# Performance work log

Measured on AMD Instinct MI355X. Metric: run time of the kernel, lower is better.

## Reference

```python
import jax, jax.numpy as jnp
import numpy as np

N, E, B, D, H, L = 50000, 800000, 16, 64, 128, 2


def _lin(h, w, b):
    return h @ w + b


def _scatter_mean(v, idx, n):
    s = jax.ops.segment_sum(v, idx, num_segments=n)
    c = jax.ops.segment_sum(jnp.ones((v.shape[0],), v.dtype), idx, num_segments=n)
    return s / jnp.maximum(c, 1.0)[:, None]


def setup_inputs() -> dict:
    key = jax.random.key(0)
    ks = iter(jax.random.split(key, 40))

    def p(*shape):
        return jax.random.normal(next(ks), shape, dtype=jnp.float32) * 0.05

    inp = {
        "x": jax.random.normal(next(ks), (N, D), dtype=jnp.float32),
        "edge_attr": jax.random.normal(next(ks), (E, D), dtype=jnp.float32),
        "u": jax.random.normal(next(ks), (B, D), dtype=jnp.float32),
        "e_w1": p(L, 4 * D, H), "e_b1": p(L, H),
        "e_w2": p(L, H, H), "e_b2": p(L, H),
        "e_w3": p(L, H, D), "e_b3": p(L, D),
        "n1_w1": p(L, 2 * D, H), "n1_b1": p(L, H),
        "n1_w2": p(L, H, H), "n1_b2": p(L, H),
        "n2_w1": p(L, D + H + D, H), "n2_b1": p(L, H),
        "n2_w2": p(L, H, D), "n2_b2": p(L, D),
        "g_w1": p(L, 3 * D, H), "g_b1": p(L, H),
        "g_w2": p(L, H, D), "g_b2": p(L, D),
        "edge_index": jax.random.randint(next(ks), (2, E), 0, N, dtype=jnp.int32),
        "batch": jnp.sort(jax.random.randint(next(ks), (N,), 0, B, dtype=jnp.int32)),
    }
    return inp


def _forward(x, edge_attr, u, params, edge_index, batch):
    row, col = edge_index[0], edge_index[1]
    eb = batch[row]  # [E] graph id per edge
    x0, e0, u0 = x, edge_attr, u
    for l in range(L):
        (e_w1, e_b1, e_w2, e_b2, e_w3, e_b3,
         n1_w1, n1_b1, n1_w2, n1_b2,
         n2_w1, n2_b1, n2_w2, n2_b2,
         g_w1, g_b1, g_w2, g_b2) = [pm[l] for pm in params]
        # Edge model: [E, e+2n+u] -> MLP -> [E, D]
        h = jnp.concatenate([x[row], x[col], edge_attr, u[eb]], axis=1)
        h = jax.nn.relu(_lin(h, e_w1, e_b1))
        h = jax.nn.relu(_lin(h, e_w2, e_b2))
        edge_attr = _lin(h, e_w3, e_b3)
        # Node model: gather src node + edge, MLP1, scatter_mean onto dest, MLP2
        se = jnp.concatenate([x[row], edge_attr], axis=1)  # [E, 2D]
        se = _lin(jax.nn.relu(_lin(se, n1_w1, n1_b1)), n1_w2, n1_b2)
        agg = _scatter_mean(se, col, N)  # [N, H]
        xh = jnp.concatenate([x, agg, u[batch]], axis=1)
        x = _lin(jax.nn.relu(_lin(xh, n2_w1, n2_b1)), n2_w2, n2_b2)
        # Global model: per-graph means of updated nodes/edges
        e_agg = _scatter_mean(edge_attr, eb, B)
        n_agg = _scatter_mean(x, batch, B)
        uh = jnp.concatenate([u, n_agg, e_agg], axis=1)
        u = _lin(jax.nn.relu(_lin(uh, g_w1, g_b1)), g_w2, g_b2)
    return x + x0, edge_attr + e0, u + u0


def reference(x, edge_attr, u, e_w1, e_b1, e_w2, e_b2, e_w3, e_b3, n1_w1, n1_b1, n1_w2, n1_b2, n2_w1, n2_b1, n2_w2, n2_b2, g_w1, g_b1, g_w2, g_b2, edge_index, batch):
    params = (e_w1, e_b1, e_w2, e_b2, e_w3, e_b3,
              n1_w1, n1_b1, n1_w2, n1_b2,
              n2_w1, n2_b1, n2_w2, n2_b2,
              g_w1, g_b1, g_w2, g_b2)
    return _forward(x, edge_attr, u, params, edge_index, batch)
```

## Files before the change

### kernel.cpp

```cpp
#include <hip/hip_runtime.h>

#define N_NODES 50000
#define E_EDGES 800000
#define NG 16
#define DD 64
#define HH 128
#define NB_SCAN 49

typedef __attribute__((ext_vector_type(8))) __bf16 bf16x8;
typedef __attribute__((ext_vector_type(4))) float f32x4;
typedef unsigned int uint;
typedef unsigned short ushort;
typedef __attribute__((ext_vector_type(4))) uint uint4v;

#define MFMA16(a,b,c) __builtin_amdgcn_mfma_f32_16x16x32_bf16((a),(b),(c),0,0,0)

__device__ __forceinline__ ushort f2bf(float f){
  uint u = __builtin_bit_cast(uint, f);
  u += 0x7fffu + ((u >> 16) & 1u);
  return (ushort)(u >> 16);
}
__device__ __forceinline__ uint pk2(float a, float b){
  return (uint)f2bf(a) | ((uint)f2bf(b) << 16);
}
__device__ __forceinline__ float bflo(uint u){ return __builtin_bit_cast(float, u << 16); }
__device__ __forceinline__ float bfhi(uint u){ return __builtin_bit_cast(float, u & 0xffff0000u); }

__device__ __forceinline__ bf16x8 ldfrag(const char* base, int row, int byteoff){
  uint4v v = *(const uint4v*)(base + row*256 + (byteoff ^ ((row & 7) << 4)));
  return __builtin_bit_cast(bf16x8, v);
}
__device__ __forceinline__ uint4v ld_chunk(const char* base, int row, int c16){
  return *(const uint4v*)(base + row*256 + ((c16*16) ^ ((row & 7) << 4)));
}
__device__ __forceinline__ void st_h(char* base, int row, int col, float v){
  *(ushort*)(base + row*256 + ((col*2) ^ ((row & 7) << 4))) = f2bf(v);
}
__device__ __forceinline__ void st_chunk(char* base, int row, int c16, uint4v v){
  *(uint4v*)(base + row*256 + ((c16*16) ^ ((row & 7) << 4))) = v;
}
__device__ __forceinline__ bf16x8 ldfrag128(const char* base, int row, int byteoff){
  uint4v v = *(const uint4v*)(base + row*128 + (byteoff ^ ((row & 7) << 4)));
  return __builtin_bit_cast(bf16x8, v);
}
__device__ __forceinline__ void st_chunk128(char* base, int row, int c16, uint4v v){
  *(uint4v*)(base + row*128 + ((c16*16) ^ ((row & 7) << 4))) = v;
}
__device__ __forceinline__ void pack16_128(char* dst, int r, int c16, const float* src){
  float4 lo = *(const float4*)src;
  float4 hi = *(const float4*)(src + 4);
  uint4v v; v.x = pk2(lo.x, lo.y); v.y = pk2(lo.z, lo.w);
  v.z = pk2(hi.x, hi.y); v.w = pk2(hi.z, hi.w);
  st_chunk128(dst, r, c16, v);
}

__device__ __forceinline__ void stage_b(char* sB, const ushort* wt,
                                        int Nout, int Ktot, int koff, int t, int stride){
  for (int task = t; task < Nout*16; task += stride){
    int n = task >> 4, c = task & 15;
    uint4v v = *(const uint4v*)(wt + (long)n*Ktot + koff + c*8);
    st_chunk(sB, n, c, v);
  }
}
__device__ __forceinline__ void pack16(char* dst, int r, int c16, const float* src){
  float4 lo = *(const float4*)src;
  float4 hi = *(const float4*)(src + 4);
  uint4v v; v.x = pk2(lo.x, lo.y); v.y = pk2(lo.z, lo.w);
  v.z = pk2(hi.x, hi.y); v.w = pk2(hi.z, hi.w);
  st_chunk(dst, r, c16, v);
}
template<int NT>
__device__ __forceinline__ void gemm_acc(const char* A, const char* B,
                                         int wv, int l15, int lhi, f32x4* acc){
  #pragma unroll
  for (int kt = 0; kt < 4; ++kt){
    bf16x8 a = ldfrag(A, wv*16 + l15, kt*64 + lhi*16);
    #pragma unroll
    for (int n = 0; n < NT; ++n){
      bf16x8 bb = ldfrag(B, n*16 + l15, kt*64 + lhi*16);
      acc[n] = MFMA16(a, bb, acc[n]);
    }
  }
}
template<int NT, bool RELU>
__device__ __forceinline__ void epi_lds(char* dst, const f32x4* acc, const float* bias,
                                        int wv, int l15, int lhi){
  #pragma unroll
  for (int n = 0; n < NT; ++n){
    float bv = bias[n*16 + l15];
    #pragma unroll
    for (int j = 0; j < 4; ++j){
      int r = wv*16 + lhi*4 + j;
      float v = acc[n][j] + bv;
      if (RELU) v = fmaxf(v, 0.f);
      st_h(dst, r, n*16 + l15, v);
    }
  }
}

__global__ void pack_weights(const float* __restrict__ e1, const float* __restrict__ e2,
                             const float* __restrict__ e3, const float* __restrict__ n12,
                             const float* __restrict__ n21, const float* __restrict__ n22,
                             ushort* __restrict__ out){
  int idx = blockIdx.x * 256 + threadIdx.x;
  int l = idx / 114688, r = idx % 114688;
  const float* src; int K, N, off;
  if      (r <  32768){ src = e1;  K = 256; N = 128; off = 0; }
  else if (r <  49152){ src = e2;  K = 128; N = 128; off = 32768; }
  else if (r <  57344){ src = e3;  K = 128; N = 64;  off = 49152; }
  else if (r <  73728){ src = n12; K = 128; N = 128; off = 57344; }
  else if (r < 106496){ src = n21; K = 256; N = 128; off = 73728; }
  else                { src = n22; K = 128; N = 64;  off = 106496; }
  int q = r - off; int k = q / N; int n = q % N;
  out[(long)l*139264 + off + n*K + k] = f2bf(src[(long)l*K*N + q]);
}

__global__ void make_wc(const float* __restrict__ n1w1, const float* __restrict__ ew3,
                        const float* __restrict__ n1b1, const float* __restrict__ eb3,
                        ushort* __restrict__ packed, float* __restrict__ biasc){
  int l = blockIdx.x, t = threadIdx.x;
  const float* W1 = n1w1 + (long)l*128*128;
  const float* W3 = ew3 + (long)l*128*64;
  ushort* wc = packed + (long)l*139264 + 114688;
  for (int i = t; i < 8192; i += 256){
    int k = i >> 7, n = i & 127;
    wc[n*192 + k] = f2bf(W1[k*128 + n]);
  }
  for (int i = t; i < 16384; i += 256){
    int k2 = i >> 7, n = i & 127;
    float s = 0.f;
    for (int m = 0; m < 64; ++m) s += W3[k2*64 + m] * W1[(64 + m)*128 + n];
    wc[n*192 + 64 + k2] = f2bf(s);
  }
  if (t < 128){
    float s = n1b1[l*128 + t];
    for (int m = 0; m < 64; ++m) s += eb3[l*64 + m] * W1[(64 + m)*128 + t];
    biasc[l*128 + t] = s;
  }
}

__global__ void hist_kernel(const int* __restrict__ edge_index, const int* __restrict__ batch,
                            int* __restrict__ deg, float* __restrict__ cnt_eb){
  __shared__ float h[NG];
  int t = threadIdx.x;
  if (t < NG) h[t] = 0.f;
  __syncthreads();
  int e = blockIdx.x * 256 + t;
  if (e < E_EDGES){
    atomicAdd(deg + edge_index[E_EDGES + e], 1);
    atomicAdd(&h[batch[edge_index[e]]], 1.f);
  }
  __syncthreads();
  if (t < NG) atomicAdd(cnt_eb + t, h[t]);
}
__global__ void count_nodes_kernel(const int* __restrict__ batch, float* __restrict__ cnt_b){
  __shared__ float h[NG];
  int t = threadIdx.x;
  if (t < NG) h[t] = 0.f;
  __syncthreads();
  int n = blockIdx.x * 256 + t;
  if (n < N_NODES) atomicAdd(&h[batch[n]], 1.f);
  __syncthreads();
  if (t < NG) atomicAdd(cnt_b + t, h[t]);
}
__global__ void scan_a(const int* __restrict__ deg, int* __restrict__ bsum){
  __shared__ int red[1024];
  int i = blockIdx.x*1024 + threadIdx.x;
  red[threadIdx.x] = (i < N_NODES) ? deg[i] : 0;
  __syncthreads();
  for (int s = 512; s > 0; s >>= 1){
    if ((int)threadIdx.x < s) red[threadIdx.x] += red[threadIdx.x + s];
    __syncthreads();
  }
  if (threadIdx.x == 0) bsum[blockIdx.x] = red[0];
}
__global__ void scan_b(const int* __restrict__ bsum, int* __restrict__ bbase){
  if (threadIdx.x == 0){
    int run = 0;
    for (int b = 0; b < NB_SCAN; ++b){ int v = bsum[b]; bbase[b] = run; run += v; }
  }
}
__global__ void scan_c(const int* __restrict__ deg, const int* __restrict__ bbase,
                       int* __restrict__ off, int* __restrict__ cursor){
  __shared__ int sc[1024];
  int i = blockIdx.x*1024 + threadIdx.x;
  int v = (i < N_NODES) ? deg[i] : 0;
  sc[threadIdx.x] = v;
  __syncthreads();
  for (int d = 1; d < 1024; d <<= 1){
    int add = ((int)threadIdx.x >= d) ? sc[threadIdx.x - d] : 0;
    __syncthreads();
    sc[threadIdx.x] += add;
    __syncthreads();
  }
  if (i < N_NODES){
    int ex = sc[threadIdx.x] - v + bbase[blockIdx.x];
    off[i] = ex; cursor[i] = ex;
  }
}
__global__ void fill_kernel(const int* __restrict__ edge_index, int* __restrict__ cursor,
                            int* __restrict__ pos){
  int e = blockIdx.x*256 + threadIdx.x;
  if (e < E_EDGES){
    int c = edge_index[E_EDGES + e];
    pos[e] = atomicAdd(&cursor[c], 1);
  }
}

__global__ __launch_bounds__(256, 3) void k123_kernel(
    const float* __restrict__ x_cur, const float* e_cur,
    const float* __restrict__ u_cur,
    const int* __restrict__ ei, const int* __restrict__ batch,
    const ushort* __restrict__ w1t, const ushort* __restrict__ w2t,
    const float* __restrict__ be1, const float* __restrict__ be2,
    ushort* h2g)
{
  __shared__ __align__(16) char lds[49152];
  __shared__ int sRow[128], sCol[128], sEb[128];
  char* A  = lds;
  char* B  = lds + 16384;
  char* OV = lds + 16384;
  const int t = threadIdx.x;
  const int wv = t >> 6, l15 = t & 15, lhi = (t >> 4) & 3;
  const int ebase = blockIdx.x * 128;

  if (t < 128){
    int r = ei[ebase + t];
    sRow[t] = r; sCol[t] = ei[E_EDGES + ebase + t]; sEb[t] = batch[r];
  }
  __syncthreads();

  f32x4 acc[2][8];
  #pragma unroll
  for (int m = 0; m < 2; ++m)
    #pragma unroll
    for (int n = 0; n < 8; ++n) acc[m][n] = f32x4{0,0,0,0};

  for (int c = 0; c < 4; ++c){
    #pragma unroll
    for (int it = 0; it < 4; ++it){
      int task = t + it*256, r = task >> 3, c16 = task & 7;
      const float* s;
      if      (c == 0) s = x_cur + (long)sRow[r]*DD + c16*8;
      else if (c == 1) s = x_cur + (long)sCol[r]*DD + c16*8;
      else if (c == 2) s = e_cur + (long)(ebase + r)*DD + c16*8;
      else             s = u_cur + (long)sEb[r]*DD + c16*8;
      pack16_128(A, r, c16, s);
    }
    #pragma unroll
    for (int it = 0; it < 4; ++it){
      int task = t + it*256, n = task >> 3, c16 = task & 7;
      st_chunk128(B, n, c16, *(const uint4v*)(w1t + (long)n*256 + c*64 + c16*8));
    }
    __syncthreads();
    #pragma unroll
    for (int kt = 0; kt < 2; ++kt){
      bf16x8 a0 = ldfrag128(A, wv*32 + l15,      kt*64 + lhi*16);
      bf16x8 a1 = ldfrag128(A, wv*32 + 16 + l15, kt*64 + lhi*16);
      #pragma unroll
      for (int n = 0; n < 8; ++n){
        bf16x8 bb = ldfrag128(B, n*16 + l15, kt*64 + lhi*16);
        acc[0][n] = MFMA16(a0, bb, acc[0][n]);
        acc[1][n] = MFMA16(a1, bb, acc[1][n]);
      }
    }
    __syncthreads();
  }
  #pragma unroll
  for (int m = 0; m < 2; ++m)
    #pragma unroll
    for (int n = 0; n < 8; ++n){
      int col = n*16 + l15;
      float bv = be1[col];
      #pragma unroll
      for (int j = 0; j < 4; ++j)
        st_h(OV, wv*32 + m*16 + lhi*4 + j, col, fmaxf(acc[m][n][j] + bv, 0.f));
    }
  __syncthreads();

  #pragma unroll
  for (int m = 0; m < 2; ++m)
    #pragma unroll
    for (int n = 0; n < 8; ++n) acc[m][n] = f32x4{0,0,0,0};
  for (int kc = 0; kc < 2; ++kc){
    #pragma unroll
    for (int it = 0; it < 4; ++it){
      int task = t + it*256, n = task >> 3, c16 = task & 7;
      st_chunk128(A, n, c16, *(const uint4v*)(w2t + (long)n*128 + kc*64 + c16*8));
    }
    __syncthreads();
    #pragma unroll
    for (int kt = 0; kt < 2; ++kt){
      bf16x8 a0 = ldfrag(OV, wv*32 + l15,      kc*128 + kt*64 + lhi*16);
      bf16x8 a1 = ldfrag(OV, wv*32 + 16 + l15, kc*128 + kt*64 + lhi*16);
      #pragma unroll
      for (int n = 0; n < 8; ++n){
        bf16x8 bb = ldfrag128(A, n*16 + l15, kt*64 + lhi*16);
        acc[0][n] = MFMA16(a0, bb, acc[0][n]);
        acc[1][n] = MFMA16(a1, bb, acc[1][n]);
      }
    }
    __syncthreads();
  }
  #pragma unroll
  for (int m = 0; m < 2; ++m)
    #pragma unroll
    for (int n = 0; n < 8; ++n){
      int col = n*16 + l15;
      float bv = be2[col];
      #pragma unroll
      for (int j = 0; j < 4; ++j)
        st_h(OV, wv*32 + m*16 + lhi*4 + j, col, fmaxf(acc[m][n][j] + bv, 0.f));
    }
  __syncthreads();
  #pragma unroll
  for (int it = 0; it < 8; ++it){
    int task = t + it*256, r = task >> 4, c16 = task & 15;
    *(uint4v*)(h2g + (long)(ebase + r)*HH + c16*8) = ld_chunk(OV, r, c16);
  }
}

template<bool CSR>
__global__ __launch_bounds__(256, 3) void k45_kernel(
    const float* __restrict__ x_cur, const ushort* h2g,
    const int* __restrict__ ei, const int* __restrict__ batch,
    const int* __restrict__ pos_arr,
    const ushort* __restrict__ w3t, const ushort* __restrict__ wct,
    const ushort* __restrict__ w5t,
    const float* __restrict__ be3, const float* __restrict__ biasc,
    const float* __restrict__ bn12,
    float* e_outf, const float* __restrict__ e_resid,
    ushort* __restrict__ se_buf, float* __restrict__ agg_sum,
    float* __restrict__ e_agg, int has_resid)
{
  __shared__ __align__(16) char lds[49152];
  __shared__ float sEagg[NG*DD];
  __shared__ int sIdx[128];
  char* A  = lds;
  char* B  = lds + 16384;
  char* B2 = lds + 32768;
  char* OV = lds + 16384;
  const int t = threadIdx.x;
  const int wv = t >> 6, l15 = t & 15, lhi = (t >> 4) & 3;
  const int ebase = blockIdx.x * 128;

  if (t < 128) sIdx[t] = ei[ebase + t];
  for (int i = t; i < NG*DD; i += 256) sEagg[i] = 0.f;
  __syncthreads();

  f32x4 acc4[2][8], acc3[2][4];
  #pragma unroll
  for (int m = 0; m < 2; ++m){
    #pragma unroll
    for (int n = 0; n < 8; ++n) acc4[m][n] = f32x4{0,0,0,0};
    #pragma unroll
    for (int n = 0; n < 4; ++n) acc3[m][n] = f32x4{0,0,0,0};
  }

  for (int c = 0; c < 3; ++c){
    if (c == 0){
      #pragma unroll
      for (int it = 0; it < 4; ++it){
        int task = t + it*256, r = task >> 3, c16 = task & 7;
        pack16_128(A, r, c16, x_cur + (long)sIdx[r]*DD + c16*8);
      }
      #pragma unroll
      for (int it = 0; it < 4; ++it){
        int task = t + it*256, n = task >> 4, c16 = task & 15;
        st_chunk(B2, n, c16, *(const uint4v*)(w3t + (long)n*128 + c16*8));
      }
    } else {
      #pragma unroll
      for (int it = 0; it < 4; ++it){
        int task = t + it*256, r = task >> 3, c16 = task & 7;
        st_chunk128(A, r, c16,
            *(const uint4v*)(h2g + (long)(ebase + r)*HH + (c-1)*64 + c16*8));
      }
    }
    #pragma unroll
    for (int it = 0; it < 4; ++it){
      int task = t + it*256, n = task >> 3, c16 = task & 7;
      st_chunk128(B, n, c16, *(const uint4v*)(wct + (long)n*192 + c*64 + c16*8));
    }
    __syncthreads();
    #pragma unroll
    for (int kt = 0; kt < 2; ++kt){
      bf16x8 a0 = ldfrag128(A, wv*32 + l15,      kt*64 + lhi*16);
      bf16x8 a1 = ldfrag128(A, wv*32 + 16 + l15, kt*64 + lhi*16);
      #pragma unroll
      for (int n = 0; n < 8; ++n){
        bf16x8 bb = ldfrag128(B, n*16 + l15, kt*64 + lhi*16);
        acc4[0][n] = MFMA16(a0, bb, acc4[0][n]);
        acc4[1][n] = MFMA16(a1, bb, acc4[1][n]);
      }
      if (c >= 1){
        #pragma unroll
        for (int n = 0; n < 4; ++n){
          bf16x8 b2 = ldfrag(B2, n*16 + l15, (c-1)*128 + kt*64 + lhi*16);
          acc3[0][n] = MFMA16(a0, b2, acc3[0][n]);
          acc3[1][n] = MFMA16(a1, b2, acc3[1][n]);
        }
      }
    }
    __syncthreads();
  }

  #pragma unroll
  for (int m = 0; m < 2; ++m)
    #pragma unroll
    for (int n = 0; n < 4; ++n){
      int col = n*16 + l15;
      float bv = be3[col];
      #pragma unroll
      for (int j = 0; j < 4; ++j){
        int row = wv*32 + m*16 + lhi*4 + j;
        float v = acc3[m][n][j] + bv;
        long eg = (long)(ebase + row)*DD + col;
        e_outf[eg] = has_resid ? (v + e_resid[eg]) : v;
        int eb = batch[ei[ebase + row]];
        atomicAdd(&sEagg[eb*DD + col], v);
      }
    }
  #pragma unroll
  for (int m = 0; m < 2; ++m)
    #pragma unroll
    for (int n = 0; n < 8; ++n){
      int col = n*16 + l15;
      float bv = biasc[col];
      #pragma unroll
      for (int j = 0; j < 4; ++j)
        st_h(OV, wv*32 + m*16 + lhi*4 + j, col, fmaxf(acc4[m][n][j] + bv, 0.f));
    }
  #pragma unroll
  for (int it = 0; it < 4; ++it){
    int task = t + it*256, n = task >> 3, c16 = task & 7;
    st_chunk128(A, n, c16, *(const uint4v*)(w5t + (long)n*128 + c16*8));
  }
  if (t < 128) sIdx[t] = CSR ? pos_arr[ebase + t] : ei[E_EDGES + ebase + t];
  __syncthreads();

  f32x4 acc5[2][8];
  #pragma unroll
  for (int m = 0; m < 2; ++m)
    #pragma unroll
    for (int n = 0; n < 8; ++n) acc5[m][n] = f32x4{0,0,0,0};
  #pragma unroll
  for (int kt = 0; kt < 2; ++kt){
    bf16x8 a0 = ldfrag(OV, wv*32 + l15,      kt*64 + lhi*16);
    bf16x8 a1 = ldfrag(OV, wv*32 + 16 + l15, kt*64 + lhi*16);
    #pragma unroll
    for (int n = 0; n < 8; ++n){
      bf16x8 bb = ldfrag128(A, n*16 + l15, kt*64 + lhi*16);
      acc5[0][n] = MFMA16(a0, bb, acc5[0][n]);
      acc5[1][n] = MFMA16(a1, bb, acc5[1][n]);
    }
  }
  __syncthreads();
  #pragma unroll
  for (int it = 0; it < 4; ++it){
    int task = t + it*256, n = task >> 3, c16 = task & 7;
    st_chunk128(A, n, c16, *(const uint4v*)(w5t + (long)n*128 + 64 + c16*8));
  }
  __syncthreads();
  #pragma unroll
  for (int kt = 0; kt < 2; ++kt){
    bf16x8 a0 = ldfrag(OV, wv*32 + l15,      128 + kt*64 + lhi*16);
    bf16x8 a1 = ldfrag(OV, wv*32 + 16 + l15, 128 + kt*64 + lhi*16);
    #pragma unroll
    for (int n = 0; n < 8; ++n){
      bf16x8 bb = ldfrag128(A, n*16 + l15, kt*64 + lhi*16);
      acc5[0][n] = MFMA16(a0, bb, acc5[0][n]);
      acc5[1][n] = MFMA16(a1, bb, acc5[1][n]);
    }
  }
  __syncthreads();

  if (CSR){
    #pragma unroll
    for (int m = 0; m < 2; ++m)
      #pragma unroll
      for (int n = 0; n < 8; ++n){
        int col = n*16 + l15;
        float bv = bn12[col];
        #pragma unroll
        for (int j = 0; j < 4; ++j)
          st_h(OV, wv*32 + m*16 + lhi*4 + j, col, acc5[m][n][j] + bv);
      }
    __syncthreads();
    #pragma unroll
    for (int it = 0; it < 8; ++it){
      int task = t + it*256, r = task >> 4, c16 = task & 15;
      *(uint4v*)(se_buf + (long)sIdx[r]*HH + c16*8) = ld_chunk(OV, r, c16);
    }
  } else {
    #pragma unroll
    for (int m = 0; m < 2; ++m)
      #pragma unroll
      for (int n = 0; n < 8; ++n){
        int col = n*16 + l15;
        float bv = bn12[col];
        #pragma unroll
        for (int j = 0; j < 4; ++j){
          int row = wv*32 + m*16 + lhi*4 + j;
          atomicAdd(agg_sum + (long)sIdx[row]*HH + col, acc5[m][n][j] + bv);
        }
      }
    __syncthreads();
  }
  for (int i = t; i < NG*DD; i += 256) atomicAdd(e_agg + i, sEagg[i]);
}

template<bool CSR>
__global__ __launch_bounds__(256, 2) void node_kernel(
    const float* __restrict__ x_cur, const float* __restrict__ u_cur,
    const float* __restrict__ x_resid, const int* __restrict__ batch,
    const ushort* __restrict__ se_buf, const int* __restrict__ deg,
    const int* __restrict__ off, const float* __restrict__ agg_sum,
    const ushort* __restrict__ w_n21, const ushort* __restrict__ w_n22,
    const float* __restrict__ b_n21, const float* __restrict__ b_n22,
    float* __restrict__ x_out, float* __restrict__ n_agg, int has_resid)
{
  __shared__ __align__(16) char sA[16384];
  __shared__ __align__(16) char sB[32768];
  __shared__ __align__(16) char sH[16384];
  __shared__ int sBat[64], sDeg[64], sOff[64];
  __shared__ float sRinv[64];
  __shared__ float sNagg[NG*DD];

  const int t = threadIdx.x;
  const int wv = t >> 6, ln = t & 63, l15 = ln & 15, lhi = ln >> 4;
  const int n0 = blockIdx.x * 64;

  if (t < 64){
    int nd = n0 + t;
    int ok = nd < N_NODES;
    sBat[t] = ok ? batch[nd] : 0;
    int d = ok ? deg[nd] : 0;
    sDeg[t] = d;
    sOff[t] = ok ? off[nd] : 0;
    sRinv[t] = 1.f / fmaxf((float)d, 1.f);
  }
  for (int i = t; i < NG*DD; i += 256) sNagg[i] = 0.f;
  __syncthreads();

  float s[32];
  const int r4 = t >> 2, q = t & 3;
  if (CSR){
    #pragma unroll
    for (int k = 0; k < 32; ++k) s[k] = 0.f;
    int d = sDeg[r4], o = sOff[r4];
    for (int i = 0; i < d; ++i){
      const ushort* src = se_buf + (long)(o + i)*HH + q*32;
      #pragma unroll
      for (int c = 0; c < 4; ++c){
        uint4v v = *(const uint4v*)(src + c*8);
        #pragma unroll
        for (int jj = 0; jj < 4; ++jj){
          s[c*8 + jj*2]     += bflo(v[jj]);
          s[c*8 + jj*2 + 1] += bfhi(v[jj]);
        }
      }
    }
    float riv = sRinv[r4];
    #pragma unroll
    for (int k = 0; k < 32; ++k) s[k] *= riv;
  }

  f32x4 acc[8];
  #pragma unroll
  for (int n = 0; n < 8; ++n) acc[n] = f32x4{0.f,0.f,0.f,0.f};

  for (int half = 0; half < 2; ++half){
    if (CSR){
      for (int task = t; task < 512; task += 256){
        int r = task >> 3, c = task & 7;
        int nd = n0 + r;
        bool ok = nd < N_NODES;
        float4 lo = {0,0,0,0}, hi = {0,0,0,0};
        if (ok){
          const float* src = (half == 0) ? (x_cur + (long)nd*DD + c*8)
                                         : (u_cur + (long)sBat[r]*DD + c*8);
          lo = *(const float4*)src; hi = *(const float4*)(src + 4);
        }
        uint4v v; v.x = pk2(lo.x, lo.y); v.y = pk2(lo.z, lo.w);
        v.z = pk2(hi.x, hi.y); v.w = pk2(hi.z, hi.w);
        st_chunk(sA, r, (half == 0) ? c : (8 + c), v);
      }
      if ((half == 0 && q < 2) || (half == 1 && q >= 2)){
        int cbase = (half == 0) ? (8 + q*4) : ((q - 2)*4);
        #pragma unroll
        for (int cc = 0; cc < 4; ++cc){
          uint4v v;
          v.x = pk2(s[cc*8+0], s[cc*8+1]); v.y = pk2(s[cc*8+2], s[cc*8+3]);
          v.z = pk2(s[cc*8+4], s[cc*8+5]); v.w = pk2(s[cc*8+6], s[cc*8+7]);
          st_chunk(sA, r4, cbase + cc, v);
        }
      }
    } else {
      for (int task = t; task < 1024; task += 256){
        int r = task >> 4, c = task & 15;
        int nd = n0 + r;
        bool ok = nd < N_NODES;
        float scale = 1.f;
        const float* src;
        if (half == 0){
          if (c < 8) src = x_cur + (long)nd*DD + c*8;
          else { src = agg_sum + (long)nd*HH + (c-8)*8; scale = sRinv[r]; }
        } else {
          if (c < 8){ src = agg_sum + (long)nd*HH + 64 + c*8; scale = sRinv[r]; }
          else src = u_cur + (long)sBat[r]*DD + (c-8)*8;
        }
        float4 lo = {0,0,0,0}, hi = {0,0,0,0};
        if (ok){ lo = *(const float4*)src; hi = *(const float4*)(src + 4); }
        uint4v v; v.x = pk2(lo.x*scale, lo.y*scale); v.y = pk2(lo.z*scale, lo.w*scale);
        v.z = pk2(hi.x*scale, hi.y*scale); v.w = pk2(hi.z*scale, hi.w*scale);
        st_chunk(sA, r, c, v);
      }
    }
    stage_b(sB, w_n21, 128, 256, half*128, t, 256);
    __syncthreads();
    gemm_acc<8>(sA, sB, wv, l15, lhi, acc);
    __syncthreads();
  }
  epi_lds<8, true>(sH, acc, b_n21, wv, l15, lhi);
  stage_b(sB, w_n22, 64, 128, 0, t, 256);
  __syncthreads();

  f32x4 acc2[4];
  #pragma unroll
  for (int n = 0; n < 4; ++n) acc2[n] = f32x4{0.f,0.f,0.f,0.f};
  gemm_acc<4>(sH, sB, wv, l15, lhi, acc2);

  #pragma unroll
  for (int n = 0; n < 4; ++n){
    float bv = b_n22[n*16 + l15];
    #pragma unroll
    for (int j = 0; j < 4; ++j){
      int r = wv*16 + lhi*4 + j;
      int nd = n0 + r;
      if (nd < N_NODES){
        int col = n*16 + l15;
        float v = acc2[n][j] + bv;
        long xg = (long)nd*DD + col;
        x_out[xg] = has_resid ? (v + x_resid[xg]) : v;
        atomicAdd(&sNagg[sBat[r]*DD + col], v);
      }
    }
  }
  __syncthreads();
  for (int i = t; i < NG*DD; i += 256) atomicAdd(n_agg + i, sNagg[i]);
}

__global__ void global_kernel(const float* __restrict__ u_cur, const float* __restrict__ n_agg,
                              const float* __restrict__ e_agg, const float* __restrict__ cnt_b,
                              const float* __restrict__ cnt_e,
                              const float* __restrict__ g_w1, const float* __restrict__ g_b1,
                              const float* __restrict__ g_w2, const float* __restrict__ g_b2,
                              const float* __restrict__ u_resid, float* __restrict__ u_out,
                              int has_resid)
{
// ... 127 lines not shown
```

Before: 1.910 ms.

## Prefetch next K-chunk into registers and use lgkm-only barriers in edge kernels

The two edge-path kernels now load the next gathered activation chunk and weight chunk from global memory into registers while the current chunk's MFMA work runs. They also replace __syncthreads with a barrier that waits only on LDS counters, so outstanding global loads can stay in flight across the barrier. The k45 kernel precomputes the edge's graph id and destination index into shared memory once, instead of re-reading batch[ei[...]] per element in the epilogue, and drops some redundant barriers. The trade-off is higher register pressure from the prefetch buffers, which may reduce occupancy under the launch bounds. The weaker barrier is also a correctness risk if any global-to-LDS dependency relied on the full sync; packing row | batch<<16 assumes node ids fit in 16 bits, and N=50000 does.

```diff
diff --git a/kernel.cpp b/kernel.cpp
--- a/kernel.cpp
+++ b/kernel.cpp
@@ -26,6 +26,11 @@
 __device__ __forceinline__ float bflo(uint u){ return __builtin_bit_cast(float, u << 16); }
 __device__ __forceinline__ float bfhi(uint u){ return __builtin_bit_cast(float, u & 0xffff0000u); }
 
+__device__ __forceinline__ void lds_barrier(){
+  asm volatile("s_waitcnt lgkmcnt(0)" ::: "memory");
+  __builtin_amdgcn_s_barrier();
+}
+
 __device__ __forceinline__ bf16x8 ldfrag(const char* base, int row, int byteoff){
   uint4v v = *(const uint4v*)(base + row*256 + (byteoff ^ ((row & 7) << 4)));
   return __builtin_bit_cast(bf16x8, v);
@@ -45,13 +50,6 @@
 }
 __device__ __forceinline__ void st_chunk128(char* base, int row, int c16, uint4v v){
   *(uint4v*)(base + row*128 + ((c16*16) ^ ((row & 7) << 4))) = v;
-}
-__device__ __forceinline__ void pack16_128(char* dst, int r, int c16, const float* src){
-  float4 lo = *(const float4*)src;
-  float4 hi = *(const float4*)(src + 4);
-  uint4v v; v.x = pk2(lo.x, lo.y); v.y = pk2(lo.z, lo.w);
-  v.z = pk2(hi.x, hi.y); v.w = pk2(hi.z, hi.w);
-  st_chunk128(dst, r, c16, v);
 }
 
 __device__ __forceinline__ void stage_b(char* sB, const ushort* wt,
@@ -61,13 +59,6 @@
     uint4v v = *(const uint4v*)(wt + (long)n*Ktot + koff + c*8);
     st_chunk(sB, n, c, v);
   }
-}
-__device__ __forceinline__ void pack16(char* dst, int r, int c16, const float* src){
-  float4 lo = *(const float4*)src;
-  float4 hi = *(const float4*)(src + 4);
-  uint4v v; v.x = pk2(lo.x, lo.y); v.y = pk2(lo.z, lo.w);
-  v.z = pk2(hi.x, hi.y); v.w = pk2(hi.z, hi.w);
-  st_chunk(dst, r, c16, v);
 }
 template<int NT>
 __device__ __forceinline__ void gemm_acc(const char* A, const char* B,
@@ -230,13 +221,9 @@
   }
   __syncthreads();
 
-  f32x4 acc[2][8];
-  #pragma unroll
-  for (int m = 0; m < 2; ++m)
-    #pragma unroll
-    for (int n = 0; n < 8; ++n) acc[m][n] = f32x4{0,0,0,0};
-
-  for (int c = 0; c < 4; ++c){
+  float4 gr[8];
+  uint4v wr[4];
+  auto GLOAD = [&](int c){
     #pragma unroll
     for (int it = 0; it < 4; ++it){
       int task = t + it*256, r = task >> 3, c16 = task & 7;
@@ -245,14 +232,55 @@
       else if (c == 1) s = x_cur + (long)sCol[r]*DD + c16*8;
       else if (c == 2) s = e_cur + (long)(ebase + r)*DD + c16*8;
       else             s = u_cur + (long)sEb[r]*DD + c16*8;
-      pack16_128(A, r, c16, s);
-    }
+      gr[2*it] = *(const float4*)s; gr[2*it+1] = *(const float4*)(s + 4);
+    }
+  };
+  auto ASTORE = [&](){
+    #pragma unroll
+    for (int it = 0; it < 4; ++it){
+      int task = t + it*256, r = task >> 3, c16 = task & 7;
+      uint4v v;
+      v.x = pk2(gr[2*it].x, gr[2*it].y);     v.y = pk2(gr[2*it].z, gr[2*it].w);
+      v.z = pk2(gr[2*it+1].x, gr[2*it+1].y); v.w = pk2(gr[2*it+1].z, gr[2*it+1].w);
+      st_chunk128(A, r, c16, v);
+    }
+  };
+  auto W1LOAD = [&](int c){
     #pragma unroll
     for (int it = 0; it < 4; ++it){
       int task = t + it*256, n = task >> 3, c16 = task & 7;
-      st_chunk128(B, n, c16, *(const uint4v*)(w1t + (long)n*256 + c*64 + c16*8));
-    }
-    __syncthreads();
+      wr[it] = *(const uint4v*)(w1t + (long)n*256 + c*64 + c16*8);
+    }
+  };
+  auto W2LOAD = [&](int kc){
+    #pragma unroll
+    for (int it = 0; it < 4; ++it){
+      int task = t + it*256, n = task >> 3, c16 = task & 7;
+      wr[it] = *(const uint4v*)(w2t + (long)n*128 + kc*64 + c16*8);
+    }
+  };
+  auto BSTORE = [&](char* dst){
+    #pragma unroll
+    for (int it = 0; it < 4; ++it){
+      int task = t + it*256, n = task >> 3, c16 = task & 7;
+      st_chunk128(dst, n, c16, wr[it]);
+    }
+  };
+
+  f32x4 acc[2][8];
+  #pragma unroll
+  for (int m = 0; m < 2; ++m)
+    #pragma unroll
+    for (int n = 0; n < 8; ++n) acc[m][n] = f32x4{0,0,0,0};
+
+  GLOAD(0); W1LOAD(0);
+
+  #pragma unroll
+  for (int c = 0; c < 4; ++c){
+    ASTORE(); BSTORE(B);
+    if (c < 3){ GLOAD(c + 1); W1LOAD(c + 1); }
+    else      { W2LOAD(0); }
+    lds_barrier();
     #pragma unroll
     for (int kt = 0; kt < 2; ++kt){
       bf16x8 a0 = ldfrag128(A, wv*32 + l15,      kt*64 + lhi*16);
@@ -264,7 +292,7 @@
         acc[1][n] = MFMA16(a1, bb, acc[1][n]);
       }
     }
-    __syncthreads();
+    lds_barrier();
   }
   #pragma unroll
   for (int m = 0; m < 2; ++m)
@@ -276,19 +304,16 @@
       for (int j = 0; j < 4; ++j)
         st_h(OV, wv*32 + m*16 + lhi*4 + j, col, fmaxf(acc[m][n][j] + bv, 0.f));
     }
-  __syncthreads();
 
   #pragma unroll
   for (int m = 0; m < 2; ++m)
     #pragma unroll
     for (int n = 0; n < 8; ++n) acc[m][n] = f32x4{0,0,0,0};
+  #pragma unroll
   for (int kc = 0; kc < 2; ++kc){
-    #pragma unroll
-    for (int it = 0; it < 4; ++it){
-      int task = t + it*256, n = task >> 3, c16 = task & 7;
-      st_chunk128(A, n, c16, *(const uint4v*)(w2t + (long)n*128 + kc*64 + c16*8));
-    }
-    __syncthreads();
+    BSTORE(A);
+    if (kc == 0) W2LOAD(1);
+    lds_barrier();
     #pragma unroll
     for (int kt = 0; kt < 2; ++kt){
       bf16x8 a0 = ldfrag(OV, wv*32 + l15,      kc*128 + kt*64 + lhi*16);
@@ -300,7 +325,7 @@
         acc[1][n] = MFMA16(a1, bb, acc[1][n]);
       }
     }
-    __syncthreads();
+    lds_barrier();
   }
   #pragma unroll
   for (int m = 0; m < 2; ++m)
@@ -312,7 +337,7 @@
       for (int j = 0; j < 4; ++j)
         st_h(OV, wv*32 + m*16 + lhi*4 + j, col, fmaxf(acc[m][n][j] + bv, 0.f));
     }
-  __syncthreads();
+  lds_barrier();
   #pragma unroll
   for (int it = 0; it < 8; ++it){
     int task = t + it*256, r = task >> 4, c16 = task & 15;
@@ -335,7 +360,8 @@
 {
   __shared__ __align__(16) char lds[49152];
   __shared__ float sEagg[NG*DD];
-  __shared__ int sIdx[128];
+  __shared__ int sRow[128];
+  __shared__ int sDst[128];
   char* A  = lds;
   char* B  = lds + 16384;
   char* B2 = lds + 32768;
@@ -344,10 +370,91 @@
   const int wv = t >> 6, l15 = t & 15, lhi = (t >> 4) & 3;
   const int ebase = blockIdx.x * 128;
 
-  if (t < 128) sIdx[t] = ei[ebase + t];
+  if (t < 128){
+    int r = ei[ebase + t];
+    sDst[t] = CSR ? pos_arr[ebase + t] : ei[E_EDGES + ebase + t];
+    sRow[t] = r | (batch[r] << 16);
+  }
   for (int i = t; i < NG*DD; i += 256) sEagg[i] = 0.f;
   __syncthreads();
 
+  float4 gr[8];
+  uint4v hr[4], wr[4], b2r[4];
+  auto GLOADX = [&](){
+    #pragma unroll
+    for (int it = 0; it < 4; ++it){
+      int task = t + it*256, r = task >> 3, c16 = task & 7;
+      const float* s = x_cur + (long)(sRow[r] & 0xffff)*DD + c16*8;
+      gr[2*it] = *(const float4*)s; gr[2*it+1] = *(const float4*)(s + 4);
+    }
+  };
+  auto ASTOREX = [&](){
+    #pragma unroll
+    for (int it = 0; it < 4; ++it){
+      int task = t + it*256, r = task >> 3, c16 = task & 7;
+      uint4v v;
+      v.x = pk2(gr[2*it].x, gr[2*it].y);     v.y = pk2(gr[2*it].z, gr[2*it].w);
+      v.z = pk2(gr[2*it+1].x, gr[2*it+1].y); v.w = pk2(gr[2*it+1].z, gr[2*it+1].w);
+      st_chunk128(A, r, c16, v);
+    }
+  };
+  auto HLOAD = [&](int half){
+    #pragma unroll
+    for (int it = 0; it < 4; ++it){
+      int task = t + it*256, r = task >> 3, c16 = task & 7;
+      hr[it] = *(const uint4v*)(h2g + (long)(ebase + r)*HH + half*64 + c16*8);
+    }
+  };
+  auto ASTOREH = [&](){
+    #pragma unroll
+    for (int it = 0; it < 4; ++it){
+      int task = t + it*256, r = task >> 3, c16 = task & 7;
+      st_chunk128(A, r, c16, hr[it]);
+    }
+  };
+  auto WCLOAD = [&](int c){
+    #pragma unroll
+    for (int it = 0; it < 4; ++it){
+      int task = t + it*256, n = task >> 3, c16 = task & 7;
+      wr[it] = *(const uint4v*)(wct + (long)n*192 + c*64 + c16*8);
+    }
+  };
+  auto W5LOAD = [&](int kc){
+    #pragma unroll
+    for (int it = 0; it < 4; ++it){
+      int task = t + it*256, n = task >> 3, c16 = task & 7;
+      wr[it] = *(const uint4v*)(w5t + (long)n*128 + kc*64 + c16*8);
+    }
+  };
+  auto WSTORE = [&](){
+    #pragma unroll
+    for (int it = 0; it < 4; ++it){
+      int task = t + it*256, n = task >> 3, c16 = task & 7;
+      st_chunk128(B, n, c16, wr[it]);
+    }
+  };
+  auto WSTORE_A = [&](){
+    #pragma unroll
+    for (int it = 0; it < 4; ++it){
+      int task = t + it*256, n = task >> 3, c16 = task & 7;
+      st_chunk128(A, n, c16, wr[it]);
+    }
+  };
+  auto B2LOAD = [&](){
+    #pragma unroll
+    for (int it = 0; it < 4; ++it){
+      int task = t + it*256, n = task >> 4, c16 = task & 15;
+      b2r[it] = *(const uint4v*)(w3t + (long)n*128 + c16*8);
+    }
+  };
+  auto B2STORE = [&](){
+    #pragma unroll
+    for (int it = 0; it < 4; ++it){
+      int task = t + it*256, n = task >> 4, c16 = task & 15;
+      st_chunk(B2, n, c16, b2r[it]);
+    }
+  };
+
   f32x4 acc4[2][8], acc3[2][4];
   #pragma unroll
   for (int m = 0; m < 2; ++m){
@@ -357,32 +464,17 @@
     for (int n = 0; n < 4; ++n) acc3[m][n] = f32x4{0,0,0,0};
   }
 
+  GLOADX(); WCLOAD(0); B2LOAD();
+
+  #pragma unroll
   for (int c = 0; c < 3; ++c){
-    if (c == 0){
-      #pragma unroll
-      for (int it = 0; it < 4; ++it){
-        int task = t + it*256, r = task >> 3, c16 = task & 7;
-        pack16_128(A, r, c16, x_cur + (long)sIdx[r]*DD + c16*8);
-      }
-      #pragma unroll
-      for (int it = 0; it < 4; ++it){
-        int task = t + it*256, n = task >> 4, c16 = task & 15;
-        st_chunk(B2, n, c16, *(const uint4v*)(w3t + (long)n*128 + c16*8));
-      }
-    } else {
-      #pragma unroll
-      for (int it = 0; it < 4; ++it){
-        int task = t + it*256, r = task >> 3, c16 = task & 7;
-        st_chunk128(A, r, c16,
-            *(const uint4v*)(h2g + (long)(ebase + r)*HH + (c-1)*64 + c16*8));
-      }
-    }
-    #pragma unroll
-    for (int it = 0; it < 4; ++it){
-      int task = t + it*256, n = task >> 3, c16 = task & 7;
-      st_chunk128(B, n, c16, *(const uint4v*)(wct + (long)n*192 + c*64 + c16*8));
-    }
-    __syncthreads();
+    if (c == 0){ ASTOREX(); B2STORE(); }
+    else       { ASTOREH(); }
+    WSTORE();
+    if (c == 0){ HLOAD(0); WCLOAD(1); }
+    else if (c == 1){ HLOAD(1); WCLOAD(2); }
+    else { W5LOAD(0); }
+    lds_barrier();
     #pragma unroll
     for (int kt = 0; kt < 2; ++kt){
       bf16x8 a0 = ldfrag128(A, wv*32 + l15,      kt*64 + lhi*16);
@@ -402,7 +494,7 @@
         }
       }
     }
-    __syncthreads();
+    lds_barrier();
   }
 
   #pragma unroll
@@ -417,8 +509,7 @@
         float v = acc3[m][n][j] + bv;
         long eg = (long)(ebase + row)*DD + col;
         e_outf[eg] = has_resid ? (v + e_resid[eg]) : v;
-        int eb = batch[ei[ebase + row]];
-        atomicAdd(&sEagg[eb*DD + col], v);
+        atomicAdd(&sEagg[(sRow[row] >> 16)*DD + col], v);
       }
     }
   #pragma unroll
@@ -431,13 +522,6 @@
       for (int j = 0; j < 4; ++j)
         st_h(OV, wv*32 + m*16 + lhi*4 + j, col, fmaxf(acc4[m][n][j] + bv, 0.f));
     }
-  #pragma unroll
-  for (int it = 0; it < 4; ++it){
-    int task = t + it*256, n = task >> 3, c16 = task & 7;
-    st_chunk128(A, n, c16, *(const uint4v*)(w5t + (long)n*128 + c16*8));
-  }
-  if (t < 128) sIdx[t] = CSR ? pos_arr[ebase + t] : ei[E_EDGES + ebase + t];
-  __syncthreads();
 
   f32x4 acc5[2][8];
   #pragma unroll
@@ -445,35 +529,23 @@
     #pragma unroll
     for (int n = 0; n < 8; ++n) acc5[m][n] = f32x4{0,0,0,0};
   #pragma unroll
-  for (int kt = 0; kt < 2; ++kt){
-    bf16x8 a0 = ldfrag(OV, wv*32 + l15,      kt*64 + lhi*16);
-    bf16x8 a1 = ldfrag(OV, wv*32 + 16 + l15, kt*64 + lhi*16);
-    #pragma unroll
-    for (int n = 0; n < 8; ++n){
-      bf16x8 bb = ldfrag128(A, n*16 + l15, kt*64 + lhi*16);
-      acc5[0][n] = MFMA16(a0, bb, acc5[0][n]);
-      acc5[1][n] = MFMA16(a1, bb, acc5[1][n]);
-    }
-  }
-  __syncthreads();
-  #pragma unroll
-  for (int it = 0; it < 4; ++it){
-    int task = t + it*256, n = task >> 3, c16 = task & 7;
-    st_chunk128(A, n, c16, *(const uint4v*)(w5t + (long)n*128 + 64 + c16*8));
-  }
-  __syncthreads();
-  #pragma unroll
-  for (int kt = 0; kt < 2; ++kt){
-    bf16x8 a0 = ldfrag(OV, wv*32 + l15,      128 + kt*64 + lhi*16);
-    bf16x8 a1 = ldfrag(OV, wv*32 + 16 + l15, 128 + kt*64 + lhi*16);
-    #pragma unroll
-    for (int n = 0; n < 8; ++n){
-      bf16x8 bb = ldfrag128(A, n*16 + l15, kt*64 + lhi*16);
-      acc5[0][n] = MFMA16(a0, bb, acc5[0][n]);
-      acc5[1][n] = MFMA16(a1, bb, acc5[1][n]);
-    }
-  }
-  __syncthreads();
+  for (int kc = 0; kc < 2; ++kc){
+    WSTORE_A();
+    if (kc == 0) W5LOAD(1);
+    lds_barrier();
+    #pragma unroll
+    for (int kt = 0; kt < 2; ++kt){
+      bf16x8 a0 = ldfrag(OV, wv*32 + l15,      kc*128 + kt*64 + lhi*16);
+      bf16x8 a1 = ldfrag(OV, wv*32 + 16 + l15, kc*128 + kt*64 + lhi*16);
+      #pragma unroll
+      for (int n = 0; n < 8; ++n){
+        bf16x8 bb = ldfrag128(A, n*16 + l15, kt*64 + lhi*16);
+        acc5[0][n] = MFMA16(a0, bb, acc5[0][n]);
+        acc5[1][n] = MFMA16(a1, bb, acc5[1][n]);
+      }
+    }
+    lds_barrier();
+  }
 
   if (CSR){
     #pragma unroll
@@ -486,11 +558,11 @@
         for (int j = 0; j < 4; ++j)
           st_h(OV, wv*32 + m*16 + lhi*4 + j, col, acc5[m][n][j] + bv);
       }
-    __syncthreads();
+    lds_barrier();
     #pragma unroll
     for (int it = 0; it < 8; ++it){
       int task = t + it*256, r = task >> 4, c16 = task & 15;
-      *(uint4v*)(se_buf + (long)sIdx[r]*HH + c16*8) = ld_chunk(OV, r, c16);
+      *(uint4v*)(se_buf + (long)sDst[r]*HH + c16*8) = ld_chunk(OV, r, c16);
     }
   } else {
     #pragma unroll
@@ -502,7 +574,7 @@
         #pragma unroll
         for (int j = 0; j < 4; ++j){
           int row = wv*32 + m*16 + lhi*4 + j;
-          atomicAdd(agg_sum + (long)sIdx[row]*HH + col, acc5[m][n][j] + bv);
+          atomicAdd(agg_sum + (long)sDst[row]*HH + col, acc5[m][n][j] + bv);
         }
       }
     __syncthreads();
```

New measurement: 2.001 ms. 4.7% more time.

## Pipeline k45 kernel loads via async global_load_lds with multi-slot LDS staging

Applied to the files above, without the earlier changes.

Restructures the fused edge/node-MLP kernel so weight and h2 tiles are loaded straight into LDS with asynchronous global_load_lds into four 16KB slots, overlapping the loads with the MFMA phases through explicit vmcnt waits and raw barriers. The e_w3 weights move into registers instead of LDS, and the source-node batch id is packed into the row index so the scatter no longer does a second indirect load. LDS grows to 64KB and occupancy drops from 3 to 2 blocks per CU, which may offset the latency hiding. The hand-placed waitcnt and barrier sequencing is fragile.

```diff
diff --git a/kernel.cpp b/kernel.cpp
--- a/kernel.cpp
+++ b/kernel.cpp
@@ -26,6 +26,18 @@
 __device__ __forceinline__ float bflo(uint u){ return __builtin_bit_cast(float, u << 16); }
 __device__ __forceinline__ float bfhi(uint u){ return __builtin_bit_cast(float, u & 0xffff0000u); }
 
+__device__ __forceinline__ void bar(){
+  asm volatile("s_waitcnt lgkmcnt(0)" ::: "memory");
+  __builtin_amdgcn_s_barrier();
+}
+#define VMWAIT(n) asm volatile("s_waitcnt vmcnt(" #n ")" ::: "memory")
+
+__device__ __forceinline__ void gload16(const void* g, void* l){
+  __builtin_amdgcn_global_load_lds(
+      (const __attribute__((address_space(1))) unsigned int*)g,
+      (__attribute__((address_space(3))) unsigned int*)l, 16, 0, 0);
+}
+
 __device__ __forceinline__ bf16x8 ldfrag(const char* base, int row, int byteoff){
   uint4v v = *(const uint4v*)(base + row*256 + (byteoff ^ ((row & 7) << 4)));
   return __builtin_bit_cast(bf16x8, v);
@@ -61,13 +73,6 @@
     uint4v v = *(const uint4v*)(wt + (long)n*Ktot + koff + c*8);
     st_chunk(sB, n, c, v);
   }
-}
-__device__ __forceinline__ void pack16(char* dst, int r, int c16, const float* src){
-  float4 lo = *(const float4*)src;
-  float4 hi = *(const float4*)(src + 4);
-  uint4v v; v.x = pk2(lo.x, lo.y); v.y = pk2(lo.z, lo.w);
-  v.z = pk2(hi.x, hi.y); v.w = pk2(hi.z, hi.w);
-  st_chunk(dst, r, c16, v);
 }
 template<int NT>
 __device__ __forceinline__ void gemm_acc(const char* A, const char* B,
@@ -321,7 +326,7 @@
 }
 
 template<bool CSR>
-__global__ __launch_bounds__(256, 3) void k45_kernel(
+__global__ __launch_bounds__(256, 2) void k45_kernel(
     const float* __restrict__ x_cur, const ushort* h2g,
     const int* __restrict__ ei, const int* __restrict__ batch,
     const int* __restrict__ pos_arr,
@@ -333,21 +338,54 @@
     ushort* __restrict__ se_buf, float* __restrict__ agg_sum,
     float* __restrict__ e_agg, int has_resid)
 {
-  __shared__ __align__(16) char lds[49152];
+  __shared__ __align__(16) char lds[65536];
   __shared__ float sEagg[NG*DD];
-  __shared__ int sIdx[128];
-  char* A  = lds;
-  char* B  = lds + 16384;
-  char* B2 = lds + 32768;
-  char* OV = lds + 16384;
+  __shared__ int sRow[128];
+  __shared__ int sDst[128];
+  char* S0 = lds;
+  char* S1 = lds + 16384;
+  char* S2 = lds + 32768;
+  char* S3 = lds + 49152;
+  char* OV = lds;
+  char* SE = lds + 32768;
   const int t = threadIdx.x;
-  const int wv = t >> 6, l15 = t & 15, lhi = (t >> 4) & 3;
+  const int wv = t >> 6, lane = t & 63, l15 = t & 15, lhi = (t >> 4) & 3;
   const int ebase = blockIdx.x * 128;
 
-  if (t < 128) sIdx[t] = ei[ebase + t];
+  auto GL = [&](const ushort* base, long stride, int koff, char* slot){
+    #pragma unroll
+    for (int it = 0; it < 4; ++it){
+      int q = (wv*4 + it)*64 + lane;
+      int r = q >> 3, cp = q & 7;
+      gload16(base + (long)r*stride + koff + ((cp ^ (r & 7))*8),
+              slot + (wv*4 + it)*1024);
+    }
+  };
+
+  if (t < 128){
+    int r = ei[ebase + t];
+    sDst[t] = CSR ? pos_arr[ebase + t] : ei[E_EDGES + ebase + t];
+    sRow[t] = r | (batch[r] << 16);
+  }
+  GL(wct, 192, 0, S1);
+  GL(h2g + (long)ebase*HH, HH, 0, S2);
+  GL(wct, 192, 64, S3);
+  bf16x8 b3[4][4];
+  #pragma unroll
+  for (int n = 0; n < 4; ++n)
+    #pragma unroll
+    for (int kk = 0; kk < 4; ++kk)
+      b3[n][kk] = *(const bf16x8*)(w3t + (long)(n*16 + l15)*128 + kk*32 + lhi*8);
   for (int i = t; i < NG*DD; i += 256) sEagg[i] = 0.f;
   __syncthreads();
 
+  #pragma unroll
+  for (int it = 0; it < 4; ++it){
+    int task = t + it*256, r = task >> 3, c16 = task & 7;
+    pack16_128(S0, r, c16, x_cur + (long)(sRow[r] & 0xffff)*DD + c16*8);
+  }
+  __syncthreads();
+
   f32x4 acc4[2][8], acc3[2][4];
   #pragma unroll
   for (int m = 0; m < 2; ++m){
@@ -357,32 +395,7 @@
     for (int n = 0; n < 4; ++n) acc3[m][n] = f32x4{0,0,0,0};
   }
 
-  for (int c = 0; c < 3; ++c){
-    if (c == 0){
-      #pragma unroll
-      for (int it = 0; it < 4; ++it){
-        int task = t + it*256, r = task >> 3, c16 = task & 7;
-        pack16_128(A, r, c16, x_cur + (long)sIdx[r]*DD + c16*8);
-      }
-      #pragma unroll
-      for (int it = 0; it < 4; ++it){
-        int task = t + it*256, n = task >> 4, c16 = task & 15;
-        st_chunk(B2, n, c16, *(const uint4v*)(w3t + (long)n*128 + c16*8));
-      }
-    } else {
-      #pragma unroll
-      for (int it = 0; it < 4; ++it){
-        int task = t + it*256, r = task >> 3, c16 = task & 7;
-        st_chunk128(A, r, c16,
-            *(const uint4v*)(h2g + (long)(ebase + r)*HH + (c-1)*64 + c16*8));
-      }
-    }
-    #pragma unroll
-    for (int it = 0; it < 4; ++it){
-      int task = t + it*256, n = task >> 3, c16 = task & 7;
-      st_chunk128(B, n, c16, *(const uint4v*)(wct + (long)n*192 + c*64 + c16*8));
-    }
-    __syncthreads();
+  auto MM = [&](const char* A, const char* B){
     #pragma unroll
     for (int kt = 0; kt < 2; ++kt){
       bf16x8 a0 = ldfrag128(A, wv*32 + l15,      kt*64 + lhi*16);
@@ -393,17 +406,81 @@
         acc4[0][n] = MFMA16(a0, bb, acc4[0][n]);
         acc4[1][n] = MFMA16(a1, bb, acc4[1][n]);
       }
-      if (c >= 1){
-        #pragma unroll
-        for (int n = 0; n < 4; ++n){
-          bf16x8 b2 = ldfrag(B2, n*16 + l15, (c-1)*128 + kt*64 + lhi*16);
-          acc3[0][n] = MFMA16(a0, b2, acc3[0][n]);
-          acc3[1][n] = MFMA16(a1, b2, acc3[1][n]);
-        }
-      }
-    }
-    __syncthreads();
-  }
+    }
+  };
+  auto MM3 = [&](const char* A, const char* B, int kkbase){
+    #pragma unroll
+    for (int kt = 0; kt < 2; ++kt){
+      bf16x8 a0 = ldfrag128(A, wv*32 + l15,      kt*64 + lhi*16);
+      bf16x8 a1 = ldfrag128(A, wv*32 + 16 + l15, kt*64 + lhi*16);
+      #pragma unroll
+      for (int n = 0; n < 8; ++n){
+        bf16x8 bb = ldfrag128(B, n*16 + l15, kt*64 + lhi*16);
+        acc4[0][n] = MFMA16(a0, bb, acc4[0][n]);
+        acc4[1][n] = MFMA16(a1, bb, acc4[1][n]);
+      }
+      #pragma unroll
+      for (int n = 0; n < 4; ++n){
+        acc3[0][n] = MFMA16(a0, b3[n][kkbase + kt], acc3[0][n]);
+        acc3[1][n] = MFMA16(a1, b3[n][kkbase + kt], acc3[1][n]);
+      }
+    }
+  };
+
+  MM(S0, S1);
+  bar();
+  GL(h2g + (long)ebase*HH, HH, 64, S0);
+  GL(wct, 192, 128, S1);
+  MM3(S2, S3, 0);
+  bar();
+  GL(w5t, 128, 0, S2);
+  VMWAIT(4);
+  __builtin_amdgcn_s_barrier();
+  MM3(S0, S1, 2);
+  bar();
+  #pragma unroll
+  for (int m = 0; m < 2; ++m)
+    #pragma unroll
+    for (int n = 0; n < 8; ++n){
+      int col = n*16 + l15;
+      float bv = biasc[col];
+      #pragma unroll
+      for (int j = 0; j < 4; ++j)
+        st_h(OV, wv*32 + m*16 + lhi*4 + j, col, fmaxf(acc4[m][n][j] + bv, 0.f));
+    }
+  GL(w5t, 128, 64, S3);
+  VMWAIT(4);
+  bar();
+  f32x4 acc5[2][8];
+  #pragma unroll
+  for (int m = 0; m < 2; ++m)
+    #pragma unroll
+    for (int n = 0; n < 8; ++n) acc5[m][n] = f32x4{0,0,0,0};
+  #pragma unroll
+  for (int kt = 0; kt < 2; ++kt){
+    bf16x8 a0 = ldfrag(OV, wv*32 + l15,      kt*64 + lhi*16);
+    bf16x8 a1 = ldfrag(OV, wv*32 + 16 + l15, kt*64 + lhi*16);
+    #pragma unroll
+    for (int n = 0; n < 8; ++n){
+      bf16x8 bb = ldfrag128(S2, n*16 + l15, kt*64 + lhi*16);
+      acc5[0][n] = MFMA16(a0, bb, acc5[0][n]);
+      acc5[1][n] = MFMA16(a1, bb, acc5[1][n]);
+    }
+  }
+  VMWAIT(0);
+  __builtin_amdgcn_s_barrier();
+  #pragma unroll
+  for (int kt = 0; kt < 2; ++kt){
+    bf16x8 a0 = ldfrag(OV, wv*32 + l15,      128 + kt*64 + lhi*16);
+    bf16x8 a1 = ldfrag(OV, wv*32 + 16 + l15, 128 + kt*64 + lhi*16);
+    #pragma unroll
+    for (int n = 0; n < 8; ++n){
+      bf16x8 bb = ldfrag128(S3, n*16 + l15, kt*64 + lhi*16);
+      acc5[0][n] = MFMA16(a0, bb, acc5[0][n]);
+      acc5[1][n] = MFMA16(a1, bb, acc5[1][n]);
+    }
+  }
+  bar();
 
   #pragma unroll
   for (int m = 0; m < 2; ++m)
@@ -417,64 +494,9 @@
         float v = acc3[m][n][j] + bv;
         long eg = (long)(ebase + row)*DD + col;
         e_outf[eg] = has_resid ? (v + e_resid[eg]) : v;
-        int eb = batch[ei[ebase + row]];
-        atomicAdd(&sEagg[eb*DD + col], v);
-      }
-    }
-  #pragma unroll
-  for (int m = 0; m < 2; ++m)
-    #pragma unroll
-    for (int n = 0; n < 8; ++n){
-      int col = n*16 + l15;
-      float bv = biasc[col];
-      #pragma unroll
-      for (int j = 0; j < 4; ++j)
-        st_h(OV, wv*32 + m*16 + lhi*4 + j, col, fmaxf(acc4[m][n][j] + bv, 0.f));
-    }
-  #pragma unroll
-  for (int it = 0; it < 4; ++it){
-    int task = t + it*256, n = task >> 3, c16 = task & 7;
-    st_chunk128(A, n, c16, *(const uint4v*)(w5t + (long)n*128 + c16*8));
-  }
-  if (t < 128) sIdx[t] = CSR ? pos_arr[ebase + t] : ei[E_EDGES + ebase + t];
-  __syncthreads();
-
-  f32x4 acc5[2][8];
-  #pragma unroll
-  for (int m = 0; m < 2; ++m)
-    #pragma unroll
-    for (int n = 0; n < 8; ++n) acc5[m][n] = f32x4{0,0,0,0};
-  #pragma unroll
-  for (int kt = 0; kt < 2; ++kt){
-    bf16x8 a0 = ldfrag(OV, wv*32 + l15,      kt*64 + lhi*16);
-    bf16x8 a1 = ldfrag(OV, wv*32 + 16 + l15, kt*64 + lhi*16);
-    #pragma unroll
-    for (int n = 0; n < 8; ++n){
-      bf16x8 bb = ldfrag128(A, n*16 + l15, kt*64 + lhi*16);
-      acc5[0][n] = MFMA16(a0, bb, acc5[0][n]);
-      acc5[1][n] = MFMA16(a1, bb, acc5[1][n]);
-    }
-  }
-  __syncthreads();
-  #pragma unroll
-  for (int it = 0; it < 4; ++it){
-    int task = t + it*256, n = task >> 3, c16 = task & 7;
-    st_chunk128(A, n, c16, *(const uint4v*)(w5t + (long)n*128 + 64 + c16*8));
-  }
-  __syncthreads();
-  #pragma unroll
-  for (int kt = 0; kt < 2; ++kt){
-    bf16x8 a0 = ldfrag(OV, wv*32 + l15,      128 + kt*64 + lhi*16);
-    bf16x8 a1 = ldfrag(OV, wv*32 + 16 + l15, 128 + kt*64 + lhi*16);
-    #pragma unroll
-    for (int n = 0; n < 8; ++n){
-      bf16x8 bb = ldfrag128(A, n*16 + l15, kt*64 + lhi*16);
-      acc5[0][n] = MFMA16(a0, bb, acc5[0][n]);
-      acc5[1][n] = MFMA16(a1, bb, acc5[1][n]);
-    }
-  }
-  __syncthreads();
-
+        atomicAdd(&sEagg[(sRow[row] >> 16)*DD + col], v);
+      }
+    }
   if (CSR){
     #pragma unroll
     for (int m = 0; m < 2; ++m)
@@ -484,13 +506,13 @@
         float bv = bn12[col];
         #pragma unroll
         for (int j = 0; j < 4; ++j)
-          st_h(OV, wv*32 + m*16 + lhi*4 + j, col, acc5[m][n][j] + bv);
-      }
-    __syncthreads();
+          st_h(SE, wv*32 + m*16 + lhi*4 + j, col, acc5[m][n][j] + bv);
+      }
+    bar();
     #pragma unroll
     for (int it = 0; it < 8; ++it){
       int task = t + it*256, r = task >> 4, c16 = task & 15;
-      *(uint4v*)(se_buf + (long)sIdx[r]*HH + c16*8) = ld_chunk(OV, r, c16);
+      *(uint4v*)(se_buf + (long)sDst[r]*HH + c16*8) = ld_chunk(SE, r, c16);
     }
   } else {
     #pragma unroll
@@ -502,10 +524,10 @@
         #pragma unroll
         for (int j = 0; j < 4; ++j){
           int row = wv*32 + m*16 + lhi*4 + j;
-          atomicAdd(agg_sum + (long)sIdx[row]*HH + col, acc5[m][n][j] + bv);
+          atomicAdd(agg_sum + (long)sDst[row]*HH + col, acc5[m][n][j] + bv);
         }
       }
-    __syncthreads();
+    bar();
   }
   for (int i = t; i < NG*DD; i += 256) atomicAdd(e_agg + i, sEagg[i]);
 }
```

Result: faster. 1.794 ms (-6.1%).
